# Optimization experiments

Hardware: AMD Instinct MI355X
Metric: run time of the kernel (lower is better)

Reference implementation:

```python
import jax, jax.numpy as jnp
import numpy as np

IN_DIM, H, OUT_DIM = 64, 128, 64
B, T = 1024, 512
NEG_SLOPE = 0.01
LN_EPS = 1e-5


def _mlp_layer(x, W, b, g, beta):
    h = x @ W.T + b
    h = jnp.where(h > 0, h, NEG_SLOPE * h)  # LeakyReLU
    mu = h.mean(-1, keepdims=True)
    var = h.var(-1, keepdims=True)
    return g * (h - mu) / jnp.sqrt(var + LN_EPS) + beta


def setup_inputs() -> dict:
    key = jax.random.key(0)
    ks = jax.random.split(key, 16)
    s = 1.0 / np.sqrt(H)
    return {
        "x": jax.random.normal(ks[0], (B, T, IN_DIM), jnp.float32),
        "is_init": jax.random.randint(ks[1], (B, T, 1), 0, 2) > 0,
        "hx": jax.random.normal(ks[2], (B, H), jnp.float32),
        "W1": jax.random.uniform(ks[3], (H, IN_DIM), jnp.float32, -s, s),
        "b1": jnp.zeros((H,), jnp.float32),
        "g1": jnp.ones((H,), jnp.float32),
        "beta1": jnp.zeros((H,), jnp.float32),
        "W2": jax.random.uniform(ks[4], (H, H), jnp.float32, -s, s),
        "b2": jnp.zeros((H,), jnp.float32),
        "g2": jnp.ones((H,), jnp.float32),
        "beta2": jnp.zeros((H,), jnp.float32),
        "W_ih": jax.random.uniform(ks[5], (3 * H, H), jnp.float32, -s, s),
        "W_hh": jax.random.uniform(ks[6], (3 * H, H), jnp.float32, -s, s),
        "b_ih": jax.random.uniform(ks[7], (3 * H,), jnp.float32, -s, s),
        "b_hh": jax.random.uniform(ks[8], (3 * H,), jnp.float32, -s, s),
        "W_out": jax.random.uniform(ks[9], (OUT_DIM, H), jnp.float32, -s, s),
        "b_out": jnp.zeros((OUT_DIM,), jnp.float32),
    }


def reference(x, is_init, hx, W1, b1, g1, beta1, W2, b2, g2, beta2,
              W_ih, W_hh, b_ih, b_hh, W_out, b_out):
    # MLP: two (Linear -> LeakyReLU -> LayerNorm) layers, width 128
    h = _mlp_layer(x, W1, b1, g1, beta1)
    h = _mlp_layer(h, W2, b2, g2, beta2)

    # Precompute input-side gate preactivations for all timesteps: [B,T,3H]
    gates_x = h @ W_ih.T + b_ih
    gates_x_t = jnp.swapaxes(gates_x, 0, 1)      # [T,B,3H]
    init_t = jnp.swapaxes(is_init, 0, 1)         # [T,B,1]

    def step(h_prev, inp):
        gx, init = inp
        h_prev = jnp.where(init, 0.0, h_prev)    # reset-on-init
        gh = h_prev @ W_hh.T + b_hh
        xr, xz, xn = jnp.split(gx, 3, axis=-1)
        hr, hz, hn = jnp.split(gh, 3, axis=-1)
        r = jax.nn.sigmoid(xr + hr)
        z = jax.nn.sigmoid(xz + hz)
        n = jnp.tanh(xn + r * hn)
        h_new = (1.0 - z) * n + z * h_prev
        return h_new, h_new

    hx_final, ys = jax.lax.scan(step, hx, (gates_x_t, init_t))
    y = jnp.swapaxes(ys, 0, 1)                   # [B,T,H]
    out = y @ W_out.T + b_out                    # [B,T,OUT_DIM]
    return out, hx_final
```

## Files before the change

### kernel.cpp

```cpp
#include <hip/hip_runtime.h>
#include <hip/hip_bf16.h>

#define IN_DIM 64
#define H 128
#define G3 384
#define OUT_DIM 64
#define Bb 1024
#define Tt 512
#define NEG 0.01f
#define EPSLN 1e-5f

#define CHUNK 16
#define NCHUNK (Tt / CHUNK)

typedef __bf16 bf16_t;
typedef __bf16 bf16x8 __attribute__((ext_vector_type(8)));
typedef float f32x4 __attribute__((ext_vector_type(4)));

#define GX_OFF 0
#define GXS 392
#define HA_OFF 50176
#define HAS 136
#define HPF_OFF 67584
#define HPB_OFF 69632
#define RED_OFF 73984
#define MNR_OFF 76032
#define GHB_OFF 76544
#define GHS 388
#define VEC_OFF 82752
#define INI_OFF 89152
#define SMEM_BYTES 89440

#define V_B1 0
#define V_G1 128
#define V_BE1 256
#define V_B2 384
#define V_G2 512
#define V_BE2 640
#define V_BIH 768
#define V_BHH 1152
#define V_BOUT 1536

#define MFMA(a, b, c) __builtin_amdgcn_mfma_f32_16x16x32_bf16((a), (b), (c), 0, 0, 0)

__global__ void __launch_bounds__(256, 1) gru_fused(
    const float* __restrict__ x, const int* __restrict__ is_init,
    const float* __restrict__ hx,
    const float* __restrict__ W1, const float* __restrict__ b1,
    const float* __restrict__ g1, const float* __restrict__ be1,
    const float* __restrict__ W2, const float* __restrict__ b2,
    const float* __restrict__ g2, const float* __restrict__ be2,
    const float* __restrict__ Wih, const float* __restrict__ Whh,
    const float* __restrict__ bih, const float* __restrict__ bhh,
    const float* __restrict__ Wout, const float* __restrict__ bout,
    float* __restrict__ out)
{
    extern __shared__ char smem[];
    bf16_t* GX  = (bf16_t*)(smem + GX_OFF);
    bf16_t* HA  = (bf16_t*)(smem + HA_OFF);
    float*  HPF = (float*) (smem + HPF_OFF);
    bf16_t* HPB = (bf16_t*)(smem + HPB_OFF);
    float*  RED = (float*) (smem + RED_OFF);
    float*  MNR = (float*) (smem + MNR_OFF);
    float*  GHB = (float*) (smem + GHB_OFF);
    float*  VEC = (float*) (smem + VEC_OFF);
    int*    INI = (int*)   (smem + INI_OFF);

    const int tid  = threadIdx.x;
    const int w    = tid >> 6;
    const int lane = tid & 63;
    const int ln   = lane & 15;
    const int quad = lane >> 4;
    const int b0   = blockIdx.x * 4;

    for (int i = tid; i < H; i += 256) {
        VEC[V_B1 + i] = b1[i];  VEC[V_G1 + i] = g1[i];  VEC[V_BE1 + i] = be1[i];
        VEC[V_B2 + i] = b2[i];  VEC[V_G2 + i] = g2[i];  VEC[V_BE2 + i] = be2[i];
    }
    for (int i = tid; i < G3; i += 256) {
        VEC[V_BIH + i] = bih[i];  VEC[V_BHH + i] = bhh[i];
    }
    if (tid < OUT_DIM) VEC[V_BOUT + tid] = bout[tid];
    for (int i = tid; i < 16 * HAS; i += 256) HPB[i] = (bf16_t)0.f;
    __syncthreads();
    for (int job = tid; job < 512; job += 256) {
        int b = job >> 7, j = job & 127;
        int im = is_init[(size_t)(b0 + b) * Tt];
        float v = im ? 0.f : hx[(size_t)(b0 + b) * H + j];
        HPF[b * H + j] = v;
        HPB[b * HAS + j] = (bf16_t)v;
    }
    bf16x8 whhf[6][4];
#pragma unroll
    for (int ntl = 0; ntl < 6; ++ntl) {
        int gate = ntl >> 1, sub = ntl & 1;
        int n = gate * H + w * 32 + sub * 16 + ln;
        const float* p = Whh + (size_t)n * H;
#pragma unroll
        for (int ks = 0; ks < 4; ++ks) {
            const float* q = p + ks * 32 + quad * 8;
            bf16x8 f;
#pragma unroll
            for (int j = 0; j < 8; ++j) f[j] = (bf16_t)q[j];
            whhf[ntl][ks] = f;
        }
    }
    __syncthreads();

    for (int tc = 0; tc < NCHUNK; ++tc) {
        const int t0 = tc * CHUNK;

        f32x4 vs[4][2];

        {
            bf16x8 w1f[2][2];
#pragma unroll
            for (int ntl = 0; ntl < 2; ++ntl) {
                int n = w * 32 + ntl * 16 + ln;
                const float* p = W1 + (size_t)n * IN_DIM;
#pragma unroll
                for (int ks = 0; ks < 2; ++ks) {
                    const float* q = p + ks * 32 + quad * 8;
                    bf16x8 f;
#pragma unroll
                    for (int j = 0; j < 8; ++j) f[j] = (bf16_t)q[j];
                    w1f[ntl][ks] = f;
                }
            }
#pragma unroll
            for (int mt = 0; mt < 4; ++mt) {
                const float* xr_ = x + ((size_t)(b0 + mt) * Tt + t0 + ln) * IN_DIM;
                bf16x8 a0, a1;
#pragma unroll
                for (int j = 0; j < 8; ++j) {
                    a0[j] = (bf16_t)xr_[quad * 8 + j];
                    a1[j] = (bf16_t)xr_[32 + quad * 8 + j];
                }
#pragma unroll
                for (int ntl = 0; ntl < 2; ++ntl) {
                    f32x4 c = {0.f, 0.f, 0.f, 0.f};
                    c = MFMA(a0, w1f[ntl][0], c);
                    c = MFMA(a1, w1f[ntl][1], c);
                    vs[mt][ntl] = c;
                }
            }
            float bv[2], gv[2], bev[2];
#pragma unroll
            for (int ntl = 0; ntl < 2; ++ntl) {
                int n = w * 32 + ntl * 16 + ln;
                bv[ntl] = VEC[V_B1 + n]; gv[ntl] = VEC[V_G1 + n]; bev[ntl] = VEC[V_BE1 + n];
            }
#pragma unroll
            for (int mt = 0; mt < 4; ++mt) {
#pragma unroll
                for (int reg = 0; reg < 4; ++reg) {
                    float v0 = vs[mt][0][reg] + bv[0]; v0 = v0 > 0.f ? v0 : NEG * v0;
                    float v1 = vs[mt][1][reg] + bv[1]; v1 = v1 > 0.f ? v1 : NEG * v1;
                    vs[mt][0][reg] = v0; vs[mt][1][reg] = v1;
                    float s = v0 + v1, q = v0 * v0 + v1 * v1;
#pragma unroll
                    for (int d = 1; d < 16; d <<= 1) { s += __shfl_xor(s, d); q += __shfl_xor(q, d); }
                    if (ln == 0) {
                        int rr = mt * 16 + quad * 4 + reg;
                        RED[rr * 8 + w] = s; RED[rr * 8 + 4 + w] = q;
                    }
                }
            }
            __syncthreads();
            if (tid < 64) {
                float s = RED[tid * 8] + RED[tid * 8 + 1] + RED[tid * 8 + 2] + RED[tid * 8 + 3];
                float q = RED[tid * 8 + 4] + RED[tid * 8 + 5] + RED[tid * 8 + 6] + RED[tid * 8 + 7];
                float mean = s * (1.f / H);
                float var = q * (1.f / H) - mean * mean;
                MNR[tid * 2] = mean; MNR[tid * 2 + 1] = rsqrtf(var + EPSLN);
            }
            __syncthreads();
#pragma unroll
            for (int mt = 0; mt < 4; ++mt) {
#pragma unroll
                for (int reg = 0; reg < 4; ++reg) {
                    int rr = mt * 16 + quad * 4 + reg;
                    float mean = MNR[rr * 2], rstd = MNR[rr * 2 + 1];
#pragma unroll
                    for (int ntl = 0; ntl < 2; ++ntl) {
                        int n = w * 32 + ntl * 16 + ln;
                        HA[rr * HAS + n] = (bf16_t)(gv[ntl] * (vs[mt][ntl][reg] - mean) * rstd + bev[ntl]);
                    }
                }
            }
            __syncthreads();
        }

        {
            bf16x8 w2f[2][4];
#pragma unroll
            for (int ntl = 0; ntl < 2; ++ntl) {
                int n = w * 32 + ntl * 16 + ln;
                const float* p = W2 + (size_t)n * H;
#pragma unroll
                for (int ks = 0; ks < 4; ++ks) {
                    const float* q = p + ks * 32 + quad * 8;
                    bf16x8 f;
#pragma unroll
                    for (int j = 0; j < 8; ++j) f[j] = (bf16_t)q[j];
                    w2f[ntl][ks] = f;
                }
            }
#pragma unroll
            for (int mt = 0; mt < 4; ++mt) {
                bf16x8 af[4];
#pragma unroll
                for (int ks = 0; ks < 4; ++ks)
                    af[ks] = *(const bf16x8*)(HA + (mt * 16 + ln) * HAS + ks * 32 + quad * 8);
#pragma unroll
                for (int ntl = 0; ntl < 2; ++ntl) {
                    f32x4 c = {0.f, 0.f, 0.f, 0.f};
#pragma unroll
                    for (int ks = 0; ks < 4; ++ks) c = MFMA(af[ks], w2f[ntl][ks], c);
                    vs[mt][ntl] = c;
                }
            }
            float bv[2], gv[2], bev[2];
#pragma unroll
            for (int ntl = 0; ntl < 2; ++ntl) {
                int n = w * 32 + ntl * 16 + ln;
                bv[ntl] = VEC[V_B2 + n]; gv[ntl] = VEC[V_G2 + n]; bev[ntl] = VEC[V_BE2 + n];
            }
#pragma unroll
            for (int mt = 0; mt < 4; ++mt) {
#pragma unroll
                for (int reg = 0; reg < 4; ++reg) {
                    float v0 = vs[mt][0][reg] + bv[0]; v0 = v0 > 0.f ? v0 : NEG * v0;
                    float v1 = vs[mt][1][reg] + bv[1]; v1 = v1 > 0.f ? v1 : NEG * v1;
                    vs[mt][0][reg] = v0; vs[mt][1][reg] = v1;
                    float s = v0 + v1, q = v0 * v0 + v1 * v1;
#pragma unroll
                    for (int d = 1; d < 16; d <<= 1) { s += __shfl_xor(s, d); q += __shfl_xor(q, d); }
                    if (ln == 0) {
                        int rr = mt * 16 + quad * 4 + reg;
                        RED[rr * 8 + w] = s; RED[rr * 8 + 4 + w] = q;
                    }
                }
            }
            __syncthreads();
            if (tid < 64) {
                float s = RED[tid * 8] + RED[tid * 8 + 1] + RED[tid * 8 + 2] + RED[tid * 8 + 3];
                float q = RED[tid * 8 + 4] + RED[tid * 8 + 5] + RED[tid * 8 + 6] + RED[tid * 8 + 7];
                float mean = s * (1.f / H);
                float var = q * (1.f / H) - mean * mean;
                MNR[tid * 2] = mean; MNR[tid * 2 + 1] = rsqrtf(var + EPSLN);
            }
            __syncthreads();
#pragma unroll
            for (int mt = 0; mt < 4; ++mt) {
#pragma unroll
                for (int reg = 0; reg < 4; ++reg) {
                    int rr = mt * 16 + quad * 4 + reg;
                    float mean = MNR[rr * 2], rstd = MNR[rr * 2 + 1];
#pragma unroll
                    for (int ntl = 0; ntl < 2; ++ntl) {
                        int n = w * 32 + ntl * 16 + ln;
                        HA[rr * HAS + n] = (bf16_t)(gv[ntl] * (vs[mt][ntl][reg] - mean) * rstd + bev[ntl]);
                    }
                }
            }
            __syncthreads();
        }

        for (int ntl = 0; ntl < 6; ++ntl) {
            int n = (w * 6 + ntl) * 16 + ln;
            const float* p = Wih + (size_t)n * H;
            bf16x8 bf[4];
#pragma unroll
            for (int ks = 0; ks < 4; ++ks) {
                const float* q = p + ks * 32 + quad * 8;
                bf16x8 f;
#pragma unroll
                for (int j = 0; j < 8; ++j) f[j] = (bf16_t)q[j];
                bf[ks] = f;
            }
            float bv = VEC[V_BIH + n];
#pragma unroll
            for (int mt = 0; mt < 4; ++mt) {
                bf16x8 af[4];
#pragma unroll
                for (int ks = 0; ks < 4; ++ks)
                    af[ks] = *(const bf16x8*)(HA + (mt * 16 + ln) * HAS + ks * 32 + quad * 8);
                f32x4 c = {0.f, 0.f, 0.f, 0.f};
#pragma unroll
                for (int ks = 0; ks < 4; ++ks) c = MFMA(af[ks], bf[ks], c);
#pragma unroll
                for (int reg = 0; reg < 4; ++reg)
                    GX[(mt * 16 + quad * 4 + reg) * GXS + n] = (bf16_t)(c[reg] + bv);
            }
        }
        if (tid < 68) {
            int b = tid / 17, s = tid % 17;
            int t = t0 + s;
            INI[tid] = (t < Tt) ? is_init[(size_t)(b0 + b) * Tt + t] : 0;
        }

        for (int s = 0; s < CHUNK; ++s) {
            __syncthreads();
            bf16x8 af[4];
#pragma unroll
            for (int ks = 0; ks < 4; ++ks)
                af[ks] = *(const bf16x8*)(HPB + ln * HAS + ks * 32 + quad * 8);
            f32x4 gc[6];
#pragma unroll
            for (int ntl = 0; ntl < 6; ++ntl) {
                f32x4 c = {0.f, 0.f, 0.f, 0.f};
#pragma unroll
                for (int ks = 0; ks < 4; ++ks) c = MFMA(af[ks], whhf[ntl][ks], c);
                gc[ntl] = c;
            }
            if (quad == 0) {
#pragma unroll
                for (int ntl = 0; ntl < 6; ++ntl) {
                    int gate = ntl >> 1, sub = ntl & 1;
                    int n = gate * H + w * 32 + sub * 16 + ln;
#pragma unroll
                    for (int reg = 0; reg < 4; ++reg)
                        GHB[reg * GHS + n] = gc[ntl][reg];
                }
            }
            __syncthreads();
            const int t = t0 + s;
#pragma unroll
            for (int rep = 0; rep < 2; ++rep) {
                int job = tid + rep * 256;
                int b = job >> 7, j = job & 127;
                int rrow = b * 16 + s;
                float xr = (float)GX[rrow * GXS + j];
                float xz = (float)GX[rrow * GXS + H + j];
                float xn = (float)GX[rrow * GXS + 2 * H + j];
                float hr = GHB[b * GHS + j]         + VEC[V_BHH + j];
                float hz = GHB[b * GHS + H + j]     + VEC[V_BHH + H + j];
                float hn = GHB[b * GHS + 2 * H + j] + VEC[V_BHH + 2 * H + j];
                float r = 1.f / (1.f + __expf(-(xr + hr)));
                float z = 1.f / (1.f + __expf(-(xz + hz)));
                float a = xn + r * hn;
                a = fminf(fmaxf(a, -15.f), 15.f);
                float e = __expf(-2.f * a);
                float nn = (1.f - e) / (1.f + e);
                float hp = HPF[b * H + j];
                float hnew = (1.f - z) * nn + z * hp;
                HA[rrow * HAS + j] = (bf16_t)hnew;
                float hm;
                if (t < Tt - 1) {
                    hm = INI[b * 17 + s + 1] ? 0.f : hnew;
                } else {
                    hm = hnew;
                    out[(size_t)Bb * Tt * OUT_DIM + (size_t)(b0 + b) * H + j] = hnew;
                }
                HPF[b * H + j] = hm;
                HPB[b * HAS + j] = (bf16_t)hm;
            }
        }
        __syncthreads();

        {
            int o = w * 16 + ln;
            const float* p = Wout + (size_t)o * H;
            bf16x8 wof[4];
#pragma unroll
            for (int ks = 0; ks < 4; ++ks) {
                const float* q = p + ks * 32 + quad * 8;
                bf16x8 f;
#pragma unroll
                for (int j = 0; j < 8; ++j) f[j] = (bf16_t)q[j];
                wof[ks] = f;
            }
            float bo = VEC[V_BOUT + o];
#pragma unroll
            for (int mt = 0; mt < 4; ++mt) {
                bf16x8 af[4];
#pragma unroll
                for (int ks = 0; ks < 4; ++ks)
                    af[ks] = *(const bf16x8*)(HA + (mt * 16 + ln) * HAS + ks * 32 + quad * 8);
                f32x4 c = {0.f, 0.f, 0.f, 0.f};
#pragma unroll
                for (int ks = 0; ks < 4; ++ks) c = MFMA(af[ks], wof[ks], c);
#pragma unroll
                for (int reg = 0; reg < 4; ++reg)
                    out[((size_t)(b0 + mt) * Tt + t0 + quad * 4 + reg) * OUT_DIM + o] = c[reg] + bo;
            }
        }
        __syncthreads();
    }
}

extern "C" void kernel_launch(void* const* d_in, const int* in_sizes, int n_in,
                              void* d_out, int out_size, void* d_ws, size_t ws_size,
                              hipStream_t stream) {
    const float* x      = (const float*)d_in[0];
    const int*   is_init= (const int*)  d_in[1];
    const float* hx     = (const float*)d_in[2];
    const float* W1     = (const float*)d_in[3];
    const float* b1     = (const float*)d_in[4];
    const float* g1     = (const float*)d_in[5];
    const float* be1    = (const float*)d_in[6];
    const float* W2     = (const float*)d_in[7];
    const float* b2     = (const float*)d_in[8];
    const float* g2     = (const float*)d_in[9];
    const float* be2    = (const float*)d_in[10];
    const float* Wih    = (const float*)d_in[11];
    const float* Whh    = (const float*)d_in[12];
    const float* bih    = (const float*)d_in[13];
    const float* bhh    = (const float*)d_in[14];
    const float* Wout   = (const float*)d_in[15];
    const float* bout   = (const float*)d_in[16];
    float* out = (float*)d_out;

    hipFuncSetAttribute((const void*)gru_fused,
                        hipFuncAttributeMaxDynamicSharedMemorySize, SMEM_BYTES);
    gru_fused<<<Bb / 4, 256, SMEM_BYTES, stream>>>(
        x, is_init, hx, W1, b1, g1, be1, W2, b2, g2, be2,
        Wih, Whh, bih, bhh, Wout, bout, out);
}
```

Before: 1.539 ms.

## Halve batch per block, keep GRU state in registers, preconvert weights to bf16

```diff
diff --git a/kernel.cpp b/kernel.cpp
--- a/kernel.cpp
+++ b/kernel.cpp
@@ -12,24 +12,22 @@
 
 #define CHUNK 16
 #define NCHUNK (Tt / CHUNK)
+#define BPB 2
 
 typedef __bf16 bf16_t;
 typedef __bf16 bf16x8 __attribute__((ext_vector_type(8)));
 typedef float f32x4 __attribute__((ext_vector_type(4)));
 
+#define GXS 392
 #define GX_OFF 0
-#define GXS 392
-#define HA_OFF 50176
 #define HAS 136
-#define HPF_OFF 67584
-#define HPB_OFF 69632
-#define RED_OFF 73984
-#define MNR_OFF 76032
-#define GHB_OFF 76544
-#define GHS 388
-#define VEC_OFF 82752
-#define INI_OFF 89152
-#define SMEM_BYTES 89440
+#define HA_OFF 25088
+#define HPB_OFF 33792
+#define RED_OFF 42496
+#define MNR_OFF 43520
+#define VEC_OFF 43776
+#define INI_OFF 50176
+#define SMEM_BYTES 50320
 
 #define V_B1 0
 #define V_G1 128
@@ -41,9 +39,42 @@
 #define V_BHH 1152
 #define V_BOUT 1536
 
+#define WS_W1 0
+#define WS_W2 8192
+#define WS_WIH 24576
+#define WS_WHH 73728
+#define WS_WOUT 122880
+#define WS_ELEMS 131072
+
 #define MFMA(a, b, c) __builtin_amdgcn_mfma_f32_16x16x32_bf16((a), (b), (c), 0, 0, 0)
 
-__global__ void __launch_bounds__(256, 1) gru_fused(
+template <bool WSB>
+__device__ __forceinline__ bf16x8 ldfrag(const float* pf, const bf16_t* pb) {
+    if constexpr (WSB) {
+        return *(const bf16x8*)pb;
+    } else {
+        bf16x8 f;
+#pragma unroll
+        for (int j = 0; j < 8; ++j) f[j] = (bf16_t)pf[j];
+        return f;
+    }
+}
+
+__global__ void cvt_weights(const float* __restrict__ W1, const float* __restrict__ W2,
+                            const float* __restrict__ Wih, const float* __restrict__ Whh,
+                            const float* __restrict__ Wout, bf16_t* __restrict__ ws) {
+    int i = blockIdx.x * 256 + threadIdx.x;
+    float v;
+    if (i < WS_W2) v = W1[i];
+    else if (i < WS_WIH) v = W2[i - WS_W2];
+    else if (i < WS_WHH) v = Wih[i - WS_WIH];
+    else if (i < WS_WOUT) v = Whh[i - WS_WHH];
+    else v = Wout[i - WS_WOUT];
+    ws[i] = (bf16_t)v;
+}
+
+template <bool WSB>
+__global__ void __launch_bounds__(256, 2) gru_fused(
     const float* __restrict__ x, const int* __restrict__ is_init,
     const float* __restrict__ hx,
     const float* __restrict__ W1, const float* __restrict__ b1,
@@ -53,25 +84,30 @@
     const float* __restrict__ Wih, const float* __restrict__ Whh,
     const float* __restrict__ bih, const float* __restrict__ bhh,
     const float* __restrict__ Wout, const float* __restrict__ bout,
+    const bf16_t* __restrict__ wsb,
     float* __restrict__ out)
 {
     extern __shared__ char smem[];
     bf16_t* GX  = (bf16_t*)(smem + GX_OFF);
     bf16_t* HA  = (bf16_t*)(smem + HA_OFF);
-    float*  HPF = (float*) (smem + HPF_OFF);
     bf16_t* HPB = (bf16_t*)(smem + HPB_OFF);
     float*  RED = (float*) (smem + RED_OFF);
     float*  MNR = (float*) (smem + MNR_OFF);
-    float*  GHB = (float*) (smem + GHB_OFF);
     float*  VEC = (float*) (smem + VEC_OFF);
     int*    INI = (int*)   (smem + INI_OFF);
+
+    const bf16_t* W1B  = wsb + WS_W1;
+    const bf16_t* W2B  = wsb + WS_W2;
+    const bf16_t* WihB = wsb + WS_WIH;
+    const bf16_t* WhhB = wsb + WS_WHH;
+    const bf16_t* WoB  = wsb + WS_WOUT;
 
     const int tid  = threadIdx.x;
     const int w    = tid >> 6;
     const int lane = tid & 63;
     const int ln   = lane & 15;
     const int quad = lane >> 4;
-    const int b0   = blockIdx.x * 4;
+    const int b0   = blockIdx.x * BPB;
 
     for (int i = tid; i < H; i += 256) {
         VEC[V_B1 + i] = b1[i];  VEC[V_G1 + i] = g1[i];  VEC[V_BE1 + i] = be1[i];
@@ -81,28 +117,37 @@
         VEC[V_BIH + i] = bih[i];  VEC[V_BHH + i] = bhh[i];
     }
     if (tid < OUT_DIM) VEC[V_BOUT + tid] = bout[tid];
-    for (int i = tid; i < 16 * HAS; i += 256) HPB[i] = (bf16_t)0.f;
+    for (int i = tid; i < 2 * 16 * HAS; i += 256) HPB[i] = (bf16_t)0.f;
     __syncthreads();
-    for (int job = tid; job < 512; job += 256) {
-        int b = job >> 7, j = job & 127;
+
+    float hp[2] = {0.f, 0.f};
+    if (quad < BPB) {
+        int b = quad;
         int im = is_init[(size_t)(b0 + b) * Tt];
-        float v = im ? 0.f : hx[(size_t)(b0 + b) * H + j];
-        HPF[b * H + j] = v;
-        HPB[b * HAS + j] = (bf16_t)v;
-    }
+#pragma unroll
+        for (int sub = 0; sub < 2; ++sub) {
+            int j = w * 32 + sub * 16 + ln;
+            float v = im ? 0.f : hx[(size_t)(b0 + b) * H + j];
+            hp[sub] = v;
+            HPB[b * 4 * HAS + j] = (bf16_t)v;
+        }
+    }
+    float bh[3][2];
+#pragma unroll
+    for (int g = 0; g < 3; ++g)
+#pragma unroll
+        for (int sub = 0; sub < 2; ++sub)
+            bh[g][sub] = bhh[g * H + w * 32 + sub * 16 + ln];
+
     bf16x8 whhf[6][4];
 #pragma unroll
     for (int ntl = 0; ntl < 6; ++ntl) {
         int gate = ntl >> 1, sub = ntl & 1;
         int n = gate * H + w * 32 + sub * 16 + ln;
-        const float* p = Whh + (size_t)n * H;
 #pragma unroll
         for (int ks = 0; ks < 4; ++ks) {
-            const float* q = p + ks * 32 + quad * 8;
-            bf16x8 f;
-#pragma unroll
-            for (int j = 0; j < 8; ++j) f[j] = (bf16_t)q[j];
-            whhf[ntl][ks] = f;
+            size_t off = (size_t)n * H + ks * 32 + quad * 8;
+            whhf[ntl][ks] = ldfrag<WSB>(Whh + off, WhhB + off);
         }
     }
     __syncthreads();
@@ -110,25 +155,21 @@
     for (int tc = 0; tc < NCHUNK; ++tc) {
         const int t0 = tc * CHUNK;
 
-        f32x4 vs[4][2];
+        f32x4 vs[BPB][2];
 
         {
             bf16x8 w1f[2][2];
 #pragma unroll
             for (int ntl = 0; ntl < 2; ++ntl) {
                 int n = w * 32 + ntl * 16 + ln;
-                const float* p = W1 + (size_t)n * IN_DIM;
 #pragma unroll
                 for (int ks = 0; ks < 2; ++ks) {
-                    const float* q = p + ks * 32 + quad * 8;
-                    bf16x8 f;
-#pragma unroll
-                    for (int j = 0; j < 8; ++j) f[j] = (bf16_t)q[j];
-                    w1f[ntl][ks] = f;
-                }
-            }
-#pragma unroll
-            for (int mt = 0; mt < 4; ++mt) {
+                    size_t off = (size_t)n * IN_DIM + ks * 32 + quad * 8;
+                    w1f[ntl][ks] = ldfrag<WSB>(W1 + off, W1B + off);
+                }
+            }
+#pragma unroll
+            for (int mt = 0; mt < BPB; ++mt) {
                 const float* xr_ = x + ((size_t)(b0 + mt) * Tt + t0 + ln) * IN_DIM;
                 bf16x8 a0, a1;
 #pragma unroll
@@ -151,7 +192,7 @@
                 bv[ntl] = VEC[V_B1 + n]; gv[ntl] = VEC[V_G1 + n]; bev[ntl] = VEC[V_BE1 + n];
             }
 #pragma unroll
-            for (int mt = 0; mt < 4; ++mt) {
+            for (int mt = 0; mt < BPB; ++mt) {
 #pragma unroll
                 for (int reg = 0; reg < 4; ++reg) {
                     float v0 = vs[mt][0][reg] + bv[0]; v0 = v0 > 0.f ? v0 : NEG * v0;
@@ -167,7 +208,7 @@
                 }
             }
             __syncthreads();
-            if (tid < 64) {
+            if (tid < 32) {
                 float s = RED[tid * 8] + RED[tid * 8 + 1] + RED[tid * 8 + 2] + RED[tid * 8 + 3];
                 float q = RED[tid * 8 + 4] + RED[tid * 8 + 5] + RED[tid * 8 + 6] + RED[tid * 8 + 7];
                 float mean = s * (1.f / H);
@@ -176,7 +217,7 @@
             }
             __syncthreads();
 #pragma unroll
-            for (int mt = 0; mt < 4; ++mt) {
+            for (int mt = 0; mt < BPB; ++mt) {
 #pragma unroll
                 for (int reg = 0; reg < 4; ++reg) {
                     int rr = mt * 16 + quad * 4 + reg;
@@ -196,18 +237,14 @@
 #pragma unroll
             for (int ntl = 0; ntl < 2; ++ntl) {
                 int n = w * 32 + ntl * 16 + ln;
-                const float* p = W2 + (size_t)n * H;
 #pragma unroll
                 for (int ks = 0; ks < 4; ++ks) {
-                    const float* q = p + ks * 32 + quad * 8;
-                    bf16x8 f;
-#pragma unroll
-                    for (int j = 0; j < 8; ++j) f[j] = (bf16_t)q[j];
-                    w2f[ntl][ks] = f;
-                }
-            }
-#pragma unroll
-            for (int mt = 0; mt < 4; ++mt) {
+                    size_t off = (size_t)n * H + ks * 32 + quad * 8;
+                    w2f[ntl][ks] = ldfrag<WSB>(W2 + off, W2B + off);
+                }
+            }
+#pragma unroll
+            for (int mt = 0; mt < BPB; ++mt) {
                 bf16x8 af[4];
 #pragma unroll
                 for (int ks = 0; ks < 4; ++ks)
@@ -227,7 +264,7 @@
                 bv[ntl] = VEC[V_B2 + n]; gv[ntl] = VEC[V_G2 + n]; bev[ntl] = VEC[V_BE2 + n];
             }
 #pragma unroll
-            for (int mt = 0; mt < 4; ++mt) {
+            for (int mt = 0; mt < BPB; ++mt) {
 #pragma unroll
                 for (int reg = 0; reg < 4; ++reg) {
                     float v0 = vs[mt][0][reg] + bv[0]; v0 = v0 > 0.f ? v0 : NEG * v0;
@@ -243,7 +280,7 @@
                 }
             }
             __syncthreads();
-            if (tid < 64) {
+            if (tid < 32) {
                 float s = RED[tid * 8] + RED[tid * 8 + 1] + RED[tid * 8 + 2] + RED[tid * 8 + 3];
                 float q = RED[tid * 8 + 4] + RED[tid * 8 + 5] + RED[tid * 8 + 6] + RED[tid * 8 + 7];
                 float mean = s * (1.f / H);
@@ -252,7 +289,7 @@
             }
             __syncthreads();
 #pragma unroll
-            for (int mt = 0; mt < 4; ++mt) {
+            for (int mt = 0; mt < BPB; ++mt) {
 #pragma unroll
                 for (int reg = 0; reg < 4; ++reg) {
                     int rr = mt * 16 + quad * 4 + reg;
@@ -267,34 +304,39 @@
             __syncthreads();
         }
 
-        for (int ntl = 0; ntl < 6; ++ntl) {
-            int n = (w * 6 + ntl) * 16 + ln;
-            const float* p = Wih + (size_t)n * H;
-            bf16x8 bf[4];
-#pragma unroll
-            for (int ks = 0; ks < 4; ++ks) {
-                const float* q = p + ks * 32 + quad * 8;
-                bf16x8 f;
-#pragma unroll
-                for (int j = 0; j < 8; ++j) f[j] = (bf16_t)q[j];
-                bf[ks] = f;
-            }
-            float bv = VEC[V_BIH + n];
-#pragma unroll
-            for (int mt = 0; mt < 4; ++mt) {
+#pragma unroll
+        for (int half = 0; half < 2; ++half) {
+            bf16x8 wf[3][4];
+            float bv[3];
+#pragma unroll
+            for (int k3 = 0; k3 < 3; ++k3) {
+                int n = (w * 6 + half * 3 + k3) * 16 + ln;
+                bv[k3] = VEC[V_BIH + n];
+#pragma unroll
+                for (int ks = 0; ks < 4; ++ks) {
+                    size_t off = (size_t)n * H + ks * 32 + quad * 8;
+                    wf[k3][ks] = ldfrag<WSB>(Wih + off, WihB + off);
+                }
+            }
+#pragma unroll
+            for (int mt = 0; mt < BPB; ++mt) {
                 bf16x8 af[4];
 #pragma unroll
                 for (int ks = 0; ks < 4; ++ks)
                     af[ks] = *(const bf16x8*)(HA + (mt * 16 + ln) * HAS + ks * 32 + quad * 8);
-                f32x4 c = {0.f, 0.f, 0.f, 0.f};
-#pragma unroll
-                for (int ks = 0; ks < 4; ++ks) c = MFMA(af[ks], bf[ks], c);
-#pragma unroll
-                for (int reg = 0; reg < 4; ++reg)
-                    GX[(mt * 16 + quad * 4 + reg) * GXS + n] = (bf16_t)(c[reg] + bv);
-            }
-        }
-        if (tid < 68) {
+#pragma unroll
+                for (int k3 = 0; k3 < 3; ++k3) {
+                    int n = (w * 6 + half * 3 + k3) * 16 + ln;
+                    f32x4 c = {0.f, 0.f, 0.f, 0.f};
+#pragma unroll
+                    for (int ks = 0; ks < 4; ++ks) c = MFMA(af[ks], wf[k3][ks], c);
+#pragma unroll
+                    for (int reg = 0; reg < 4; ++reg)
+                        GX[(mt * 16 + quad * 4 + reg) * GXS + n] = (bf16_t)(c[reg] + bv[k3]);
+                }
+            }
+        }
+        if (tid < BPB * 17) {
             int b = tid / 17, s = tid % 17;
             int t = t0 + s;
             INI[tid] = (t < Tt) ? is_init[(size_t)(b0 + b) * Tt + t] : 0;
@@ -302,10 +344,12 @@
 
         for (int s = 0; s < CHUNK; ++s) {
             __syncthreads();
+            const int t = t0 + s;
+            const int rp = t & 1;
             bf16x8 af[4];
 #pragma unroll
             for (int ks = 0; ks < 4; ++ks)
-                af[ks] = *(const bf16x8*)(HPB + ln * HAS + ks * 32 + quad * 8);
+                af[ks] = *(const bf16x8*)(HPB + rp * 16 * HAS + ln * HAS + ks * 32 + quad * 8);
             f32x4 gc[6];
 #pragma unroll
             for (int ntl = 0; ntl < 6; ++ntl) {
@@ -314,66 +358,51 @@
                 for (int ks = 0; ks < 4; ++ks) c = MFMA(af[ks], whhf[ntl][ks], c);
                 gc[ntl] = c;
             }
-            if (quad == 0) {
-#pragma unroll
-                for (int ntl = 0; ntl < 6; ++ntl) {
-                    int gate = ntl >> 1, sub = ntl & 1;
-                    int n = gate * H + w * 32 + sub * 16 + ln;
-#pragma unroll
-                    for (int reg = 0; reg < 4; ++reg)
-                        GHB[reg * GHS + n] = gc[ntl][reg];
-                }
-            }
-            __syncthreads();
-            const int t = t0 + s;
-#pragma unroll
-            for (int rep = 0; rep < 2; ++rep) {
-                int job = tid + rep * 256;
-                int b = job >> 7, j = job & 127;
-                int rrow = b * 16 + s;
-                float xr = (float)GX[rrow * GXS + j];
-                float xz = (float)GX[rrow * GXS + H + j];
-                float xn = (float)GX[rrow * GXS + 2 * H + j];
-                float hr = GHB[b * GHS + j]         + VEC[V_BHH + j];
-                float hz = GHB[b * GHS + H + j]     + VEC[V_BHH + H + j];
-                float hn = GHB[b * GHS + 2 * H + j] + VEC[V_BHH + 2 * H + j];
-                float r = 1.f / (1.f + __expf(-(xr + hr)));
-                float z = 1.f / (1.f + __expf(-(xz + hz)));
-                float a = xn + r * hn;
-                a = fminf(fmaxf(a, -15.f), 15.f);
-                float e = __expf(-2.f * a);
-                float nn = (1.f - e) / (1.f + e);
-                float hp = HPF[b * H + j];
-                float hnew = (1.f - z) * nn + z * hp;
-                HA[rrow * HAS + j] = (bf16_t)hnew;
-                float hm;
-                if (t < Tt - 1) {
-                    hm = INI[b * 17 + s + 1] ? 0.f : hnew;
-                } else {
-                    hm = hnew;
-                    out[(size_t)Bb * Tt * OUT_DIM + (size_t)(b0 + b) * H + j] = hnew;
-                }
-                HPF[b * H + j] = hm;
-                HPB[b * HAS + j] = (bf16_t)hm;
+            if (quad < BPB) {
+                const int b = quad;
+                bf16_t* hw = HPB + (rp ^ 1) * 16 * HAS + b * 4 * HAS;
+                const int rbase = (b * 16 + s) * GXS;
+#pragma unroll
+                for (int sub = 0; sub < 2; ++sub) {
+                    int j = w * 32 + sub * 16 + ln;
+                    float xr = (float)GX[rbase + j];
+                    float xz = (float)GX[rbase + H + j];
+                    float xn = (float)GX[rbase + 2 * H + j];
+                    float hr = gc[sub][0]     + bh[0][sub];
+                    float hz = gc[2 + sub][0] + bh[1][sub];
+                    float hn = gc[4 + sub][0] + bh[2][sub];
+                    float r = 1.f / (1.f + __expf(-(xr + hr)));
+                    float z = 1.f / (1.f + __expf(-(xz + hz)));
+                    float a = xn + r * hn;
+                    a = fminf(fmaxf(a, -15.f), 15.f);
+                    float e = __expf(-2.f * a);
+                    float nn = (1.f - e) / (1.f + e);
+                    float hnew = (1.f - z) * nn + z * hp[sub];
+                    HA[(b * 16 + s) * HAS + j] = (bf16_t)hnew;
+                    float hm;
+                    if (t < Tt - 1) {
+                        hm = INI[b * 17 + s + 1] ? 0.f : hnew;
+                    } else {
+                        hm = hnew;
+                        out[(size_t)Bb * Tt * OUT_DIM + (size_t)(b0 + b) * H + j] = hnew;
+                    }
+                    hp[sub] = hm;
+                    hw[j] = (bf16_t)hm;
+                }
             }
         }
         __syncthreads();
 
         {
             int o = w * 16 + ln;
-            const float* p = Wout + (size_t)o * H;
+            size_t ob = (size_t)o * H;
             bf16x8 wof[4];
 #pragma unroll
-            for (int ks = 0; ks < 4; ++ks) {
-                const float* q = p + ks * 32 + quad * 8;
-                bf16x8 f;
-#pragma unroll
-                for (int j = 0; j < 8; ++j) f[j] = (bf16_t)q[j];
-                wof[ks] = f;
-            }
+            for (int ks = 0; ks < 4; ++ks)
+                wof[ks] = ldfrag<WSB>(Wout + ob + ks * 32 + quad * 8, WoB + ob + ks * 32 + quad * 8);
             float bo = VEC[V_BOUT + o];
 #pragma unroll
-            for (int mt = 0; mt < 4; ++mt) {
+            for (int mt = 0; mt < BPB; ++mt) {
                 bf16x8 af[4];
 #pragma unroll
                 for (int ks = 0; ks < 4; ++ks)
@@ -412,9 +441,20 @@
     const float* bout   = (const float*)d_in[16];
     float* out = (float*)d_out;
 
-    hipFuncSetAttribute((const void*)gru_fused,
-                        hipFuncAttributeMaxDynamicSharedMemorySize, SMEM_BYTES);
-    gru_fused<<<Bb / 4, 256, SMEM_BYTES, stream>>>(
-        x, is_init, hx, W1, b1, g1, be1, W2, b2, g2, be2,
-        Wih, Whh, bih, bhh, Wout, bout, out);
+    const bool usews = (d_ws != nullptr) && (ws_size >= (size_t)(WS_ELEMS * sizeof(bf16_t)));
+    if (usews) {
+        bf16_t* ws = (bf16_t*)d_ws;
+        cvt_weights<<<WS_ELEMS / 256, 256, 0, stream>>>(W1, W2, Wih, Whh, Wout, ws);
+        hipFuncSetAttribute((const void*)gru_fused<true>,
+                            hipFuncAttributeMaxDynamicSharedMemorySize, SMEM_BYTES);
+        gru_fused<true><<<Bb / BPB, 256, SMEM_BYTES, stream>>>(
+            x, is_init, hx, W1, b1, g1, be1, W2, b2, g2, be2,
+            Wih, Whh, bih, bhh, Wout, bout, ws, out);
+    } else {
+        hipFuncSetAttribute((const void*)gru_fused<false>,
+                            hipFuncAttributeMaxDynamicSharedMemorySize, SMEM_BYTES);
+        gru_fused<false><<<Bb / BPB, 256, SMEM_BYTES, stream>>>(
+            x, is_init, hx, W1, b1, g1, be1, W2, b2, g2, be2,
+            Wih, Whh, bih, bhh, Wout, bout, nullptr, out);
+    }
 }
```

New measurement: 1.402 ms. 8.9% less time.
